# Optimization experiments

Measured on AMD Instinct MI355X. Metric: run time of the kernel, lower is better.

Reference implementation:

```python
import jax, jax.numpy as jnp
import numpy as np

HIDDEN = 1024
NUM_HEADS = 16
B, S = 2, 2048


def _mha(x, w_in, b_in, w_out, b_out, num_heads):
    # x: [..., L, E]; standard nn.MultiheadAttention math (eval mode, no dropout)
    lead = x.shape[:-2]
    L, E = x.shape[-2], x.shape[-1]
    dh = E // num_heads
    qkv = x @ w_in.T + b_in                      # [..., L, 3E]
    q, k, v = jnp.split(qkv, 3, axis=-1)
    q = q.reshape(lead + (L, num_heads, dh)) * (dh ** -0.5)
    k = k.reshape(lead + (L, num_heads, dh))
    v = v.reshape(lead + (L, num_heads, dh))
    scores = jnp.einsum('...qhd,...khd->...hqk', q, k)
    probs = jax.nn.softmax(scores, axis=-1)
    out = jnp.einsum('...hqk,...khd->...qhd', probs, v).reshape(lead + (L, E))
    return out @ w_out.T + b_out


def setup_inputs() -> dict:
    key = jax.random.key(0)
    ks = jax.random.split(key, 12)
    E = HIDDEN
    s_in = 1.0 / np.sqrt(E)
    inp = {
        'x': jax.random.normal(ks[0], (B, S, E), dtype=jnp.float32),
        'w_in_g': jax.random.normal(ks[1], (3 * E, E), dtype=jnp.float32) * s_in,
        'b_in_g': jnp.zeros((3 * E,), dtype=jnp.float32),
        'w_out_g': jax.random.normal(ks[2], (E, E), dtype=jnp.float32) * s_in,
        'b_out_g': jnp.zeros((E,), dtype=jnp.float32),
        'w_in_l': jax.random.normal(ks[3], (3 * E, E), dtype=jnp.float32) * s_in,
        'b_in_l': jnp.zeros((3 * E,), dtype=jnp.float32),
        'w_out_l': jax.random.normal(ks[4], (E, E), dtype=jnp.float32) * s_in,
        'b_out_l': jnp.zeros((E,), dtype=jnp.float32),
        'w_f': jax.random.normal(ks[5], (E, 2 * E), dtype=jnp.float32) * (1.0 / np.sqrt(2 * E)),
        'b_f': jnp.zeros((E,), dtype=jnp.float32),
    }
    return inp


def reference(x, w_in_g, b_in_g, w_out_g, b_out_g,
              w_in_l, b_in_l, w_out_l, b_out_l, w_f, b_f):
    Bn, Sn, E = x.shape
    # global full attention over the whole sequence
    g = _mha(x, w_in_g, b_in_g, w_out_g, b_out_g, NUM_HEADS)   # [B,S,E]
    # block-local attention: blocks of length num_heads along the sequence
    sub_len = NUM_HEADS
    sub_num = Sn // sub_len
    xb = x.reshape(Bn, sub_num, sub_len, E)
    l = _mha(xb, w_in_l, b_in_l, w_out_l, b_out_l, NUM_HEADS).reshape(Bn, Sn, E)
    fused = jnp.concatenate([g, l], axis=-1)                   # [B,S,2E]
    return fused @ w_f.T + b_f
```

## Files before the change

kernel.cpp:

```cpp
#include <hip/hip_runtime.h>
#include <hip/hip_bf16.h>
#include <math.h>
#include <stdint.h>

constexpr int Bz = 2;
constexpr int S  = 2048;
constexpr int E  = 1024;
constexpr int NH = 16;
constexpr int DH = 64;
constexpr int QS = 6144;
constexpr int NSPLIT = 2;
constexpr int KT_SPLIT = (S / 64) / NSPLIT;

typedef __attribute__((ext_vector_type(8))) short short8;
typedef __attribute__((ext_vector_type(4))) float f32x4;
typedef __attribute__((ext_vector_type(8))) unsigned short bf16x8;
typedef __attribute__((ext_vector_type(4))) unsigned short bf16x4;

__device__ __forceinline__ float bf2f(unsigned short u) {
    union { unsigned int i; float f; } c; c.i = ((unsigned int)u) << 16; return c.f;
}
__device__ __forceinline__ unsigned short f2bf(float f) {
    union { float f; unsigned int i; } c; c.f = f;
    unsigned int r = c.i + 0x7fffu + ((c.i >> 16) & 1u);
    return (unsigned short)(r >> 16);
}

__device__ __forceinline__ void pack4_store(unsigned short* dst,
                                            float a, float b, float c, float d) {
#if __has_builtin(__builtin_amdgcn_cvt_pk_bf16_f32)
    auto p0 = __builtin_amdgcn_cvt_pk_bf16_f32(a, b);
    auto p1 = __builtin_amdgcn_cvt_pk_bf16_f32(c, d);
    union { decltype(p0) v; unsigned int u; } c0, c1;
    c0.v = p0; c1.v = p1;
    uint2 w; w.x = c0.u; w.y = c1.u;
    *(uint2*)dst = w;
#else
    bf16x4 o = { f2bf(a), f2bf(b), f2bf(c), f2bf(d) };
    *(bf16x4*)dst = o;
#endif
}

#define GLD_LDS(g, l) __builtin_amdgcn_global_load_lds( \
    (const __attribute__((address_space(1))) void*)(g), \
    (__attribute__((address_space(3))) void*)(l), 16, 0, 0)

struct PrepArgs {
    const float* csrc[4]; unsigned short* cdst[4]; int cn[4];
    const float* wog; const float* wol;
    unsigned short* wogT; unsigned short* wolT;
    const float* wf; const float* bf; const float* bog; const float* bol;
    float* cb;
};

__global__ __launch_bounds__(256)
void prep_all(PrepArgs a)
{
    __shared__ unsigned short T[64][72];
    const int bid = blockIdx.x, t = threadIdx.x;

    if (bid < 12288) {
        int i = (bid * 256 + t) * 4;
        #pragma unroll
        for (int r = 0; r < 4; ++r) {
            if (i < a.cn[r]) {
                float4 v = *(const float4*)(a.csrc[r] + i);
                bf16x4 o = { f2bf(v.x), f2bf(v.y), f2bf(v.z), f2bf(v.w) };
                *(bf16x4*)(a.cdst[r] + i) = o;
                return;
            }
            i -= a.cn[r];
        }
        return;
    }
    if (bid < 12800) {
        const int id = bid - 12288;
        const int tj = id & 15, ti = (id >> 4) & 15, mat = id >> 8;
        const float* src = mat ? a.wol : a.wog;
        unsigned short* dst = mat ? a.wolT : a.wogT;
        #pragma unroll
        for (int r = 0; r < 4; ++r) {
            const int c = r * 256 + t;
            const int row = c >> 4, col4 = (c & 15) * 4;
            float4 v = *(const float4*)(src + (size_t)(ti * 64 + row) * 1024 + tj * 64 + col4);
            T[col4 + 0][row] = f2bf(v.x);
            T[col4 + 1][row] = f2bf(v.y);
            T[col4 + 2][row] = f2bf(v.z);
            T[col4 + 3][row] = f2bf(v.w);
        }
        __syncthreads();
        #pragma unroll
        for (int r = 0; r < 2; ++r) {
            const int c = r * 256 + t;
            const int jrow = c >> 3, ig = (c & 7) * 8;
            bf16x8 o;
            #pragma unroll
            for (int k = 0; k < 8; ++k) o[k] = T[jrow][ig + k];
            *(bf16x8*)(dst + (size_t)(tj * 64 + jrow) * 1024 + ti * 64 + ig) = o;
        }
        return;
    }
    {
        const int lane = t & 63;
        const int n = (bid - 12800) * 4 + (t >> 6);
        const float* row = a.wf + (size_t)n * 2048;
        float s = 0.f;
        #pragma unroll
        for (int i = 0; i < 16; ++i) s = fmaf(row[i * 64 + lane], a.bog[i * 64 + lane], s);
        #pragma unroll
        for (int i = 16; i < 32; ++i) s = fmaf(row[i * 64 + lane], a.bol[i * 64 + lane - 1024], s);
        #pragma unroll
        for (int off = 32; off > 0; off >>= 1) s += __shfl_xor(s, off, 64);
        if (lane == 0) a.cb[n] = a.bf[n] + s;
    }
}

__global__ __launch_bounds__(256, 2)
void gemm_bk64(const unsigned short* __restrict__ A, const unsigned short* __restrict__ W,
               const float* __restrict__ bias0, const float* __restrict__ bias1,
               unsigned short* __restrict__ C, unsigned short* __restrict__ vtout,
               unsigned short* __restrict__ vtlout,
               int M, int N, int K, int lda, int ldw, int ldc, int nsplit)
{
    __shared__ __align__(16) short As[128 * 64];
    __shared__ __align__(16) short Bs[128 * 64];
    const int t = threadIdx.x;
    const int lane = t & 63, wave = t >> 6;
    const int wm = wave & 1, wn = wave >> 1;
    const int m0 = blockIdx.y * 128, n0 = blockIdx.x * 128;
    const int lm = lane & 15, lk = lane >> 4;

    f32x4 acc[4][4] = {};

    const int row0 = t >> 3, kg0 = (t & 7) * 8;
    const unsigned short* a0 = A + (size_t)(m0 + row0) * lda + kg0;
    const unsigned short* w0 = W + (size_t)(n0 + row0) * ldw + kg0;

    for (int k0 = 0; k0 < K; k0 += 64) {
        __syncthreads();
        #pragma unroll
        for (int r = 0; r < 4; ++r)
            GLD_LDS(a0 + (size_t)(r * 32) * lda + k0, As + ((size_t)(r * 256 + wave * 64)) * 8);
        #pragma unroll
        for (int r = 0; r < 4; ++r)
            GLD_LDS(w0 + (size_t)(r * 32) * ldw + k0, Bs + ((size_t)(r * 256 + wave * 64)) * 8);
        __syncthreads();

        #pragma unroll
        for (int ks = 0; ks < 2; ++ks) {
            short8 af[4], bfr[4];
            #pragma unroll
            for (int i = 0; i < 4; ++i)
                af[i] = *(const short8*)&As[(wm * 64 + i * 16 + lm) * 64 + ks * 32 + lk * 8];
            #pragma unroll
            for (int j = 0; j < 4; ++j)
                bfr[j] = *(const short8*)&Bs[(wn * 64 + j * 16 + lm) * 64 + ks * 32 + lk * 8];
            #pragma unroll
            for (int i = 0; i < 4; ++i)
                #pragma unroll
                for (int j = 0; j < 4; ++j)
                    acc[i][j] = __builtin_amdgcn_mfma_f32_16x16x32_bf16(af[i], bfr[j], acc[i][j], 0, 0, 0);
        }
    }

    #pragma unroll
    for (int i = 0; i < 4; ++i) {
        #pragma unroll
        for (int j = 0; j < 4; ++j) {
            const int nn = n0 + wn * 64 + j * 16 + lm;
            const float bv = (nn < nsplit) ? (bias0 ? bias0[nn] : 0.f)
                                           : (bias1 ? bias1[nn - nsplit] : 0.f);
            const int mm0 = m0 + wm * 64 + i * 16 + lk * 4;
            float vv[4];
            #pragma unroll
            for (int r = 0; r < 4; ++r) {
                vv[r] = acc[i][j][r] + bv;
                C[(size_t)(mm0 + r) * ldc + nn] = f2bf(vv[r]);
            }
            if (vtout) {
                const int nl = nn - 2048;
                if (nl >= 0 && nl < 1024) {
                    const int hh = nl >> 6, dd = nl & 63;
                    const int bb = mm0 >> 11, ss = mm0 & 2047;
                    pack4_store(vtout + ((size_t)(bb * NH + hh) * 64 + dd) * S + ss,
                                vv[0], vv[1], vv[2], vv[3]);
                }
                const int nl2 = nn - 5120;
                if (nl2 >= 0) {
                    const int hh = nl2 >> 6, dd = nl2 & 63;
                    const int bb = mm0 >> 11, ss = mm0 & 2047;
                    pack4_store(vtlout + ((size_t)(bb * NH + hh) * 64 + dd) * S + ss,
                                vv[0], vv[1], vv[2], vv[3]);
                }
            }
        }
    }
}

template<typename OutT>
__global__ __launch_bounds__(256, 2)
void gemm_m64(const unsigned short* __restrict__ A, const unsigned short* __restrict__ W,
              const float* __restrict__ bias, OutT* __restrict__ C,
              int M, int N, int K, int lda, int ldw, int ldc,
              size_t sAz, size_t sWz, size_t sCz)
{
    __shared__ __align__(16) short As[64 * 32];
    __shared__ __align__(16) short Bs[128 * 32];
    const int z = blockIdx.z;
    A += z * sAz;  W += z * sWz;  C += z * sCz;

    const int t = threadIdx.x;
    const int lane = t & 63, wave = t >> 6;
    const int wm = wave & 1, wn = wave >> 1;
    const int m0 = blockIdx.y * 64, n0 = blockIdx.x * 128;
    const int lm = lane & 15, lk = lane >> 4;

    f32x4 acc[2][4] = {};

    const int rowA = t >> 2, kgA = (t & 3) * 8;
    const unsigned short* aptr = A + (size_t)(m0 + rowA) * lda + kgA;
    const unsigned short* wptr = W + (size_t)(n0 + rowA) * ldw + kgA;

    for (int k0 = 0; k0 < K; k0 += 32) {
        __syncthreads();
        GLD_LDS(aptr + k0, As + ((size_t)(wave * 64)) * 8);
        #pragma unroll
        for (int r = 0; r < 2; ++r)
            GLD_LDS(wptr + (size_t)(r * 64) * ldw + k0, Bs + ((size_t)(r * 256 + wave * 64)) * 8);
        __syncthreads();

        short8 af[2], bfr[4];
        #pragma unroll
        for (int i = 0; i < 2; ++i)
            af[i] = *(const short8*)&As[(wm * 32 + i * 16 + lm) * 32 + lk * 8];
        #pragma unroll
        for (int j = 0; j < 4; ++j)
            bfr[j] = *(const short8*)&Bs[(wn * 64 + j * 16 + lm) * 32 + lk * 8];
        #pragma unroll
        for (int i = 0; i < 2; ++i)
            #pragma unroll
            for (int j = 0; j < 4; ++j)
                acc[i][j] = __builtin_amdgcn_mfma_f32_16x16x32_bf16(af[i], bfr[j], acc[i][j], 0, 0, 0);
    }

    #pragma unroll
    for (int i = 0; i < 2; ++i) {
        #pragma unroll
        for (int j = 0; j < 4; ++j) {
            const int nn = n0 + wn * 64 + j * 16 + lm;
            const float bv = bias ? bias[nn] : 0.f;
            #pragma unroll
            for (int r = 0; r < 4; ++r) {
                const int mm = m0 + wm * 32 + i * 16 + lk * 4 + r;
                const float v = acc[i][j][r] + bv;
                const size_t idx = (size_t)mm * ldc + nn;
                if constexpr (sizeof(OutT) == 2) ((unsigned short*)C)[idx] = f2bf(v);
                else                             C[idx] = v;
            }
        }
    }
}

__global__ __launch_bounds__(256, 2)
void attn_flash(const unsigned short* __restrict__ qkv,
                const unsigned short* __restrict__ vt,
                unsigned short* __restrict__ opart, float* __restrict__ lbuf)
{
    __shared__ __align__(16) unsigned short Ks[2][64][32];
    __shared__ __align__(16) unsigned short Vs[2][64][32];
    __shared__ __align__(16) unsigned short Pt[4][2][16][64];

    const int t = threadIdx.x, lane = t & 63, wq = t >> 6;
    const int lm = lane & 15, lk = lane >> 4;
    const int bid = blockIdx.x;
    const int split = bid & 1;
    const int qb = (bid >> 1) & 15;
    const int h  = (bid >> 5) & 15;
    const int b  = bid >> 9;
    const int q0 = qb * 128 + wq * 32;

    constexpr float QSCALE = 0.125f * 1.44269504088896340736f;
    short8 qf[2][2];
    #pragma unroll
    for (int qg = 0; qg < 2; ++qg) {
        const unsigned short* qrow = qkv + ((size_t)(b * S) + q0 + qg * 16 + lm) * QS + h * DH;
        #pragma unroll
        for (int kk = 0; kk < 2; ++kk) {
            bf16x8 v = *(const bf16x8*)(qrow + kk * 32 + lk * 8);
            #pragma unroll
            for (int j = 0; j < 8; ++j)
                ((unsigned short*)&qf[qg][kk])[j] = f2bf(bf2f(v[j]) * QSCALE);
        }
    }

    short8 ones;
    #pragma unroll
    for (int j = 0; j < 8; ++j) ((unsigned short*)&ones)[j] = 0x3F80;

    const int row0 = t >> 2;
    const int sw0 = (row0 ^ (row0 >> 2)) & 3;
    const int g0 = ((t & 3) ^ sw0) * 8;
    const unsigned short* kg[2];
    const unsigned short* vg[2];
    #pragma unroll
    for (int r = 0; r < 2; ++r) {
        kg[r] = qkv + ((size_t)(b * S) + row0) * QS + E + h * 64 + r * 32 + g0;
        vg[r] = vt + ((size_t)(b * NH + h) * 64 + row0) * S + r * 32 + g0;
    }
    unsigned short* kl[2] = { &Ks[0][0][0] + (wq * 64) * 8, &Ks[0][0][0] + (256 + wq * 64) * 8 };
    unsigned short* vl[2] = { &Vs[0][0][0] + (wq * 64) * 8, &Vs[0][0][0] + (256 + wq * 64) * 8 };

    f32x4 O[2][4] = {};
    f32x4 lacc[2] = {};
    const int sw = lm & 7;
    const int fr = (lm ^ (lm >> 2)) & 3;

    for (int kt = split * KT_SPLIT; kt < (split + 1) * KT_SPLIT; ++kt) {
        __syncthreads();
        GLD_LDS(kg[0] + (size_t)kt * 64 * QS, kl[0]);
        GLD_LDS(kg[1] + (size_t)kt * 64 * QS, kl[1]);
        GLD_LDS(vg[0] + kt * 64, vl[0]);
        GLD_LDS(vg[1] + kt * 64, vl[1]);
        __syncthreads();

        f32x4 st[2][4];
        #pragma unroll
        for (int qg = 0; qg < 2; ++qg)
            #pragma unroll
            for (int jn = 0; jn < 4; ++jn)
                st[qg][jn] = (f32x4){ -16.f, -16.f, -16.f, -16.f };
        #pragma unroll
        for (int jn = 0; jn < 4; ++jn) {
            #pragma unroll
            for (int kk = 0; kk < 2; ++kk) {
                short8 kf = *(const short8*)&Ks[kk][jn * 16 + lm][(lk ^ fr) * 8];
                #pragma unroll
                for (int qg = 0; qg < 2; ++qg)
                    st[qg][jn] = __builtin_amdgcn_mfma_f32_16x16x32_bf16(kf, qf[qg][kk], st[qg][jn], 0, 0, 0);
            }
        }

        #pragma unroll
        for (int qg = 0; qg < 2; ++qg)
            #pragma unroll
            for (int jn = 0; jn < 4; ++jn) {
                const int cc = ((jn * 2 + (lk >> 1)) ^ sw) * 8 + (lk & 1) * 4;
                pack4_store(&Pt[wq][qg][lm][cc],
                            exp2f(st[qg][jn][0]), exp2f(st[qg][jn][1]),
                            exp2f(st[qg][jn][2]), exp2f(st[qg][jn][3]));
            }

        short8 pf[2][2];
        #pragma unroll
        for (int qg = 0; qg < 2; ++qg) {
            pf[qg][0] = *(const short8*)&Pt[wq][qg][lm][((lk + 0) ^ sw) * 8];
            pf[qg][1] = *(const short8*)&Pt[wq][qg][lm][((lk + 4) ^ sw) * 8];
        }

        #pragma unroll
        for (int qg = 0; qg < 2; ++qg)
            #pragma unroll
            for (int kk = 0; kk < 2; ++kk)
                lacc[qg] = __builtin_amdgcn_mfma_f32_16x16x32_bf16(ones, pf[qg][kk], lacc[qg], 0, 0, 0);

        #pragma unroll
        for (int jd = 0; jd < 4; ++jd) {
            #pragma unroll
            for (int kk = 0; kk < 2; ++kk) {
                short8 vf = *(const short8*)&Vs[kk][jd * 16 + lm][(lk ^ fr) * 8];
                #pragma unroll
                for (int qg = 0; qg < 2; ++qg)
                    O[qg][jd] = __builtin_amdgcn_mfma_f32_16x16x32_bf16(vf, pf[qg][kk], O[qg][jd], 0, 0, 0);
            }
        }
    }

    #pragma unroll
    for (int qg = 0; qg < 2; ++qg) {
        const int q = q0 + qg * 16 + lm;
        unsigned short* orow = opart + ((((size_t)split * Bz + b) * NH + h) * S + q) * 64;
        #pragma unroll
        for (int jd = 0; jd < 4; ++jd)
            pack4_store(orow + jd * 16 + lk * 4,
                        O[qg][jd][0], O[qg][jd][1], O[qg][jd][2], O[qg][jd][3]);
        if (lk == 0)
            lbuf[(((size_t)split * Bz + b) * NH + h) * S + q] = lacc[qg][0];
    }
}

__global__ __launch_bounds__(256)
void attn_merge(const unsigned short* __restrict__ opart, const float* __restrict__ lbuf,
                unsigned short* __restrict__ attn)
{
    const int id = blockIdx.x * 256 + threadIdx.x;
    const int d8 = id & 7;
    const int q  = (id >> 3) & (S - 1);
    const int h  = (id >> 14) & 15;
    const int b  = id >> 18;

    const size_t base0 = (((size_t)0 * Bz + b) * NH + h) * S + q;
    const size_t base1 = (((size_t)1 * Bz + b) * NH + h) * S + q;
    const float inv = 1.0f / (lbuf[base0] + lbuf[base1]);

    bf16x8 o0 = *(const bf16x8*)(opart + base0 * 64 + d8 * 8);
    bf16x8 o1 = *(const bf16x8*)(opart + base1 * 64 + d8 * 8);
    unsigned short* dst = attn + ((size_t)(b * S) + q) * 2048 + h * 64 + d8 * 8;
    #pragma unroll
    for (int j = 0; j < 8; j += 4)
        pack4_store(dst + j,
                    (bf2f(o0[j+0]) + bf2f(o1[j+0])) * inv,
                    (bf2f(o0[j+1]) + bf2f(o1[j+1])) * inv,
                    (bf2f(o0[j+2]) + bf2f(o1[j+2])) * inv,
                    (bf2f(o0[j+3]) + bf2f(o1[j+3])) * inv);
}

__global__ __launch_bounds__(256)
void attn_local_mfma(const unsigned short* __restrict__ qkvl,
                     const unsigned short* __restrict__ vtl,
                     unsigned short* __restrict__ outp)
{
    __shared__ __align__(16) unsigned short Pt[4][16][32];
    const int t = threadIdx.x, lane = t & 63, wq = t >> 6;
    const int lm = lane & 15, lk = lane >> 4;
    const int gid = blockIdx.x * 4 + wq;
    const int h   = gid & 15;
    const int sub = (gid >> 4) & 127;
    const int b   = gid >> 11;
    const int s0  = sub * 16;

    const unsigned short* base = qkvl + ((size_t)(b * S) + s0 + lm) * QS;
    f32x4 st = {};
    #pragma unroll
    for (int kk = 0; kk < 2; ++kk) {
        short8 kf = *(const short8*)(base + E + h * 64 + kk * 32 + lk * 8);
        short8 qf = *(const short8*)(base +     h * 64 + kk * 32 + lk * 8);
        st = __builtin_amdgcn_mfma_f32_16x16x32_bf16(kf, qf, st, 0, 0, 0);
    }

    constexpr float SC = 0.125f * 1.44269504088896340736f;
    float tt[4];
    #pragma unroll
    for (int r = 0; r < 4; ++r) tt[r] = st[r] * SC;
    float mx = fmaxf(fmaxf(tt[0], tt[1]), fmaxf(tt[2], tt[3]));
    mx = fmaxf(mx, __shfl_xor(mx, 16, 64));
    mx = fmaxf(mx, __shfl_xor(mx, 32, 64));
    float p[4], l = 0.f;
    #pragma unroll
    for (int r = 0; r < 4; ++r) { p[r] = exp2f(tt[r] - mx); l += p[r]; }
    l += __shfl_xor(l, 16, 64);
    l += __shfl_xor(l, 32, 64);
    const float inv = 1.0f / l;

    pack4_store(&Pt[wq][lm][lk * 4], p[0], p[1], p[2], p[3]);
    pack4_store(&Pt[wq][lm][16 + lk * 4], 0.f, 0.f, 0.f, 0.f);
    short8 pf = *(const short8*)&Pt[wq][lm][lk * 8];

    const unsigned short* vrow =
        vtl + (((size_t)(b * NH + h) * 64) + lm) * S + s0 + (lk & 1) * 8;
    f32x4 zero = {};
    unsigned short* dst = outp + ((size_t)(b * S) + s0 + lm) * 2048 + 1024 + h * 64 + lk * 4;
    #pragma unroll
    for (int jd = 0; jd < 4; ++jd) {
        short8 vf = *(const short8*)(vrow + (size_t)jd * 16 * S);
        f32x4 O = __builtin_amdgcn_mfma_f32_16x16x32_bf16(vf, pf, zero, 0, 0, 0);
        pack4_store(dst + jd * 16, O[0] * inv, O[1] * inv, O[2] * inv, O[3] * inv);
    }
}

extern "C" void kernel_launch(void* const* d_in, const int* in_sizes, int n_in,
                              void* d_out, int out_size, void* d_ws, size_t ws_size,
                              hipStream_t stream)
{
    const float* x       = (const float*)d_in[0];
    const float* w_in_g  = (const float*)d_in[1];
    const float* b_in_g  = (const float*)d_in[2];
    const float* w_out_g = (const float*)d_in[3];
    const float* b_out_g = (const float*)d_in[4];
    const float* w_in_l  = (const float*)d_in[5];
    const float* b_in_l  = (const float*)d_in[6];
    const float* w_out_l = (const float*)d_in[7];
    const float* b_out_l = (const float*)d_in[8];
    const float* w_f     = (const float*)d_in[9];
    const float* b_f     = (const float*)d_in[10];
    float* out = (float*)d_out;

    const int M = Bz * S;
    char* p = (char*)d_ws;
    unsigned short* xb       = (unsigned short*)p; p += (size_t)M * 1024 * 2;
    unsigned short* qkv_all  = (unsigned short*)p; p += (size_t)M * QS * 2;
    unsigned short* attn_cat = (unsigned short*)p; p += (size_t)M * 2048 * 2;
    unsigned short* win_all  = (unsigned short*)p; p += (size_t)6144 * 1024 * 2;
    unsigned short* wf_b     = (unsigned short*)p; p += (size_t)1024 * 2048 * 2;
    unsigned short* woutT    = (unsigned short*)p; p += (size_t)2 * 1024 * 1024 * 2;
    unsigned short* wcomb    = (unsigned short*)p; p += (size_t)1024 * 2048 * 2;
    unsigned short* vtbuf    = (unsigned short*)p; p += (size_t)Bz * NH * 64 * S * 2;
    unsigned short* opart    = (unsigned short*)p; p += (size_t)NSPLIT * Bz * NH * S * 64 * 2;
    float*          lbuf     = (float*)p;          p += (size_t)NSPLIT * Bz * NH * S * 4;
    float*          cb       = (float*)p;          p += 1024 * 4;

    unsigned short* vtlbuf = opart;

    dim3 blk(256);

    PrepArgs pa;
    pa.csrc[0] = x;      pa.cdst[0] = xb;                    pa.cn[0] = M * 1024;
    pa.csrc[1] = w_in_g; pa.cdst[1] = win_all;               pa.cn[1] = 3072 * 1024;
    pa.csrc[2] = w_in_l; pa.cdst[2] = win_all + 3072 * 1024; pa.cn[2] = 3072 * 1024;
    pa.csrc[3] = w_f;    pa.cdst[3] = wf_b;                  pa.cn[3] = 1024 * 2048;
    pa.wog = w_out_g; pa.wol = w_out_l;
    pa.wogT = woutT;  pa.wolT = woutT + 1024 * 1024;
    pa.wf = w_f; pa.bf = b_f; pa.bog = b_out_g; pa.bol = b_out_l; pa.cb = cb;
    prep_all<<<dim3(13056), blk, 0, stream>>>(pa);

    gemm_m64<unsigned short><<<dim3(8, 16, 2), blk, 0, stream>>>(
        wf_b, woutT, nullptr, wcomb,
        1024, 1024, 1024, 2048, 1024, 2048,
        1024, (size_t)1024 * 1024, 1024);

    gemm_bk64<<<dim3(6144 / 128, M / 128), blk, 0, stream>>>(
        xb, win_all, b_in_g, b_in_l, qkv_all, vtbuf, vtlbuf,
        M, 6144, 1024, 1024, 1024, QS, 3072);

    attn_local_mfma<<<dim3(Bz * NH * (S / 16) / 4), blk, 0, stream>>>(
        qkv_all + 3072, vtlbuf, attn_cat);

    attn_flash<<<dim3(Bz * NH * (S / 128) * NSPLIT), blk, 0, stream>>>(
        qkv_all, vtbuf, opart, lbuf);
    attn_merge<<<dim3(Bz * NH * S * 8 / 256), blk, 0, stream>>>(opart, lbuf, attn_cat);

    gemm_m64<float><<<dim3(1024 / 128, M / 64, 1), blk, 0, stream>>>(
        attn_cat, wcomb, cb, out,
        M, 1024, 2048, 2048, 2048, 1024,
        0, 0, 0);
}
```

Baseline: 312.3 us.

## Merge GEMM launches and fuse local/global attention, drop split-K merge

```diff
diff --git a/kernel.cpp b/kernel.cpp
--- a/kernel.cpp
+++ b/kernel.cpp
@@ -9,8 +9,6 @@
 constexpr int NH = 16;
 constexpr int DH = 64;
 constexpr int QS = 6144;
-constexpr int NSPLIT = 2;
-constexpr int KT_SPLIT = (S / 64) / NSPLIT;
 
 typedef __attribute__((ext_vector_type(8))) short short8;
 typedef __attribute__((ext_vector_type(4))) float f32x4;
@@ -115,19 +113,45 @@
     }
 }
 
+struct GemmFusedArgs {
+    const unsigned short* xb;    const unsigned short* win;
+    const unsigned short* wfb;   const unsigned short* woutT;
+    const float* bg;             const float* bl;
+    unsigned short* qkv;  unsigned short* vt;  unsigned short* vtl;
+    unsigned short* wcomb;
+};
+
 __global__ __launch_bounds__(256, 2)
-void gemm_bk64(const unsigned short* __restrict__ A, const unsigned short* __restrict__ W,
-               const float* __restrict__ bias0, const float* __restrict__ bias1,
-               unsigned short* __restrict__ C, unsigned short* __restrict__ vtout,
-               unsigned short* __restrict__ vtlout,
-               int M, int N, int K, int lda, int ldw, int ldc, int nsplit)
+void gemm_fused(GemmFusedArgs g)
 {
     __shared__ __align__(16) short As[128 * 64];
     __shared__ __align__(16) short Bs[128 * 64];
+
+    const int bid = blockIdx.x;
+    const unsigned short *A, *W;
+    unsigned short *C, *vt, *vtl;
+    const float *bias0, *bias1;
+    int m0, n0, lda, ldw, ldc, nsplit;
+
+    if (bid < 1536) {
+        m0 = (bid / 48) * 128;  n0 = (bid % 48) * 128;
+        A = g.xb;  W = g.win;  C = g.qkv;  vt = g.vt;  vtl = g.vtl;
+        bias0 = g.bg;  bias1 = g.bl;
+        lda = 1024;  ldw = 1024;  ldc = QS;  nsplit = 3072;
+    } else {
+        const int id = bid - 1536;
+        const int z = id >> 6;
+        m0 = ((id >> 3) & 7) * 128;  n0 = (id & 7) * 128;
+        A = g.wfb + z * 1024;
+        W = g.woutT + (size_t)z * 1024 * 1024;
+        C = g.wcomb + z * 1024;
+        vt = nullptr;  vtl = nullptr;  bias0 = nullptr;  bias1 = nullptr;
+        lda = 2048;  ldw = 1024;  ldc = 2048;  nsplit = 0;
+    }
+
     const int t = threadIdx.x;
     const int lane = t & 63, wave = t >> 6;
     const int wm = wave & 1, wn = wave >> 1;
-    const int m0 = blockIdx.y * 128, n0 = blockIdx.x * 128;
     const int lm = lane & 15, lk = lane >> 4;
 
     f32x4 acc[4][4] = {};
@@ -136,7 +160,7 @@
     const unsigned short* a0 = A + (size_t)(m0 + row0) * lda + kg0;
     const unsigned short* w0 = W + (size_t)(n0 + row0) * ldw + kg0;
 
-    for (int k0 = 0; k0 < K; k0 += 64) {
+    for (int k0 = 0; k0 < 1024; k0 += 64) {
         __syncthreads();
         #pragma unroll
         for (int r = 0; r < 4; ++r)
@@ -177,19 +201,19 @@
                 vv[r] = acc[i][j][r] + bv;
                 C[(size_t)(mm0 + r) * ldc + nn] = f2bf(vv[r]);
             }
-            if (vtout) {
+            if (vt) {
                 const int nl = nn - 2048;
                 if (nl >= 0 && nl < 1024) {
                     const int hh = nl >> 6, dd = nl & 63;
                     const int bb = mm0 >> 11, ss = mm0 & 2047;
-                    pack4_store(vtout + ((size_t)(bb * NH + hh) * 64 + dd) * S + ss,
+                    pack4_store(vt + ((size_t)(bb * NH + hh) * 64 + dd) * S + ss,
                                 vv[0], vv[1], vv[2], vv[3]);
                 }
                 const int nl2 = nn - 5120;
                 if (nl2 >= 0) {
                     const int hh = nl2 >> 6, dd = nl2 & 63;
                     const int bb = mm0 >> 11, ss = mm0 & 2047;
-                    pack4_store(vtlout + ((size_t)(bb * NH + hh) * 64 + dd) * S + ss,
+                    pack4_store(vtl + ((size_t)(bb * NH + hh) * 64 + dd) * S + ss,
                                 vv[0], vv[1], vv[2], vv[3]);
                 }
             }
@@ -262,9 +286,10 @@
 }
 
 __global__ __launch_bounds__(256, 2)
-void attn_flash(const unsigned short* __restrict__ qkv,
+void attn_fused(const unsigned short* __restrict__ qkv,
                 const unsigned short* __restrict__ vt,
-                unsigned short* __restrict__ opart, float* __restrict__ lbuf)
+                const unsigned short* __restrict__ vtl,
+                unsigned short* __restrict__ attn)
 {
     __shared__ __align__(16) unsigned short Ks[2][64][32];
     __shared__ __align__(16) unsigned short Vs[2][64][32];
@@ -272,157 +297,127 @@
 
     const int t = threadIdx.x, lane = t & 63, wq = t >> 6;
     const int lm = lane & 15, lk = lane >> 4;
-    const int bid = blockIdx.x;
-    const int split = bid & 1;
-    const int qb = (bid >> 1) & 15;
-    const int h  = (bid >> 5) & 15;
-    const int b  = bid >> 9;
-    const int q0 = qb * 128 + wq * 32;
-
-    constexpr float QSCALE = 0.125f * 1.44269504088896340736f;
-    short8 qf[2][2];
-    #pragma unroll
-    for (int qg = 0; qg < 2; ++qg) {
-        const unsigned short* qrow = qkv + ((size_t)(b * S) + q0 + qg * 16 + lm) * QS + h * DH;
-        #pragma unroll
-        for (int kk = 0; kk < 2; ++kk) {
-            bf16x8 v = *(const bf16x8*)(qrow + kk * 32 + lk * 8);
-            #pragma unroll
-            for (int j = 0; j < 8; ++j)
-                ((unsigned short*)&qf[qg][kk])[j] = f2bf(bf2f(v[j]) * QSCALE);
-        }
-    }
-
-    short8 ones;
-    #pragma unroll
-    for (int j = 0; j < 8; ++j) ((unsigned short*)&ones)[j] = 0x3F80;
-
-    const int row0 = t >> 2;
-    const int sw0 = (row0 ^ (row0 >> 2)) & 3;
-    const int g0 = ((t & 3) ^ sw0) * 8;
-    const unsigned short* kg[2];
-    const unsigned short* vg[2];
-    #pragma unroll
-    for (int r = 0; r < 2; ++r) {
-        kg[r] = qkv + ((size_t)(b * S) + row0) * QS + E + h * 64 + r * 32 + g0;
-        vg[r] = vt + ((size_t)(b * NH + h) * 64 + row0) * S + r * 32 + g0;
-    }
-    unsigned short* kl[2] = { &Ks[0][0][0] + (wq * 64) * 8, &Ks[0][0][0] + (256 + wq * 64) * 8 };
-    unsigned short* vl[2] = { &Vs[0][0][0] + (wq * 64) * 8, &Vs[0][0][0] + (256 + wq * 64) * 8 };
-
-    f32x4 O[2][4] = {};
-    f32x4 lacc[2] = {};
-    const int sw = lm & 7;
-    const int fr = (lm ^ (lm >> 2)) & 3;
-
-    for (int kt = split * KT_SPLIT; kt < (split + 1) * KT_SPLIT; ++kt) {
-        __syncthreads();
-        GLD_LDS(kg[0] + (size_t)kt * 64 * QS, kl[0]);
-        GLD_LDS(kg[1] + (size_t)kt * 64 * QS, kl[1]);
-        GLD_LDS(vg[0] + kt * 64, vl[0]);
-        GLD_LDS(vg[1] + kt * 64, vl[1]);
-        __syncthreads();
-
-        f32x4 st[2][4];
-        #pragma unroll
-        for (int qg = 0; qg < 2; ++qg)
-            #pragma unroll
-            for (int jn = 0; jn < 4; ++jn)
-                st[qg][jn] = (f32x4){ -16.f, -16.f, -16.f, -16.f };
-        #pragma unroll
-        for (int jn = 0; jn < 4; ++jn) {
+
+    if (blockIdx.x < 512) {
+        const int bid = blockIdx.x;
+        const int qb = bid & 15;
+        const int h  = (bid >> 4) & 15;
+        const int b  = bid >> 8;
+        const int q0 = qb * 128 + wq * 32;
+
+        constexpr float QSCALE = 0.125f * 1.44269504088896340736f;
+        short8 qf[2][2];
+        #pragma unroll
+        for (int qg = 0; qg < 2; ++qg) {
+            const unsigned short* qrow = qkv + ((size_t)(b * S) + q0 + qg * 16 + lm) * QS + h * DH;
             #pragma unroll
             for (int kk = 0; kk < 2; ++kk) {
-                short8 kf = *(const short8*)&Ks[kk][jn * 16 + lm][(lk ^ fr) * 8];
-                #pragma unroll
-                for (int qg = 0; qg < 2; ++qg)
-                    st[qg][jn] = __builtin_amdgcn_mfma_f32_16x16x32_bf16(kf, qf[qg][kk], st[qg][jn], 0, 0, 0);
-            }
-        }
-
-        #pragma unroll
-        for (int qg = 0; qg < 2; ++qg)
+                bf16x8 v = *(const bf16x8*)(qrow + kk * 32 + lk * 8);
+                #pragma unroll
+                for (int j = 0; j < 8; ++j)
+                    ((unsigned short*)&qf[qg][kk])[j] = f2bf(bf2f(v[j]) * QSCALE);
+            }
+        }
+
+        short8 ones;
+        #pragma unroll
+        for (int j = 0; j < 8; ++j) ((unsigned short*)&ones)[j] = 0x3F80;
+
+        const int row0 = t >> 2;
+        const int sw0 = (row0 ^ (row0 >> 2)) & 3;
+        const int g0 = ((t & 3) ^ sw0) * 8;
+        const unsigned short* kg[2];
+        const unsigned short* vg[2];
+        #pragma unroll
+        for (int r = 0; r < 2; ++r) {
+            kg[r] = qkv + ((size_t)(b * S) + row0) * QS + E + h * 64 + r * 32 + g0;
+            vg[r] = vt + ((size_t)(b * NH + h) * 64 + row0) * S + r * 32 + g0;
+        }
+        unsigned short* kl[2] = { &Ks[0][0][0] + (wq * 64) * 8, &Ks[0][0][0] + (256 + wq * 64) * 8 };
+        unsigned short* vl[2] = { &Vs[0][0][0] + (wq * 64) * 8, &Vs[0][0][0] + (256 + wq * 64) * 8 };
+
+        f32x4 O[2][4] = {};
+        f32x4 lacc[2] = {};
+        const int sw = lm & 7;
+        const int fr = (lm ^ (lm >> 2)) & 3;
+
+        for (int kt = 0; kt < 32; ++kt) {
+            __syncthreads();
+            GLD_LDS(kg[0] + (size_t)kt * 64 * QS, kl[0]);
+            GLD_LDS(kg[1] + (size_t)kt * 64 * QS, kl[1]);
+            GLD_LDS(vg[0] + kt * 64, vl[0]);
+            GLD_LDS(vg[1] + kt * 64, vl[1]);
+            __syncthreads();
+
+            f32x4 st[2][4];
+            #pragma unroll
+            for (int qg = 0; qg < 2; ++qg)
+                #pragma unroll
+                for (int jn = 0; jn < 4; ++jn)
+                    st[qg][jn] = (f32x4){ -16.f, -16.f, -16.f, -16.f };
             #pragma unroll
             for (int jn = 0; jn < 4; ++jn) {
-                const int cc = ((jn * 2 + (lk >> 1)) ^ sw) * 8 + (lk & 1) * 4;
-                pack4_store(&Pt[wq][qg][lm][cc],
-                            exp2f(st[qg][jn][0]), exp2f(st[qg][jn][1]),
-                            exp2f(st[qg][jn][2]), exp2f(st[qg][jn][3]));
-            }
-
-        short8 pf[2][2];
+                #pragma unroll
+                for (int kk = 0; kk < 2; ++kk) {
+                    short8 kf = *(const short8*)&Ks[kk][jn * 16 + lm][(lk ^ fr) * 8];
+                    #pragma unroll
+                    for (int qg = 0; qg < 2; ++qg)
+                        st[qg][jn] = __builtin_amdgcn_mfma_f32_16x16x32_bf16(kf, qf[qg][kk], st[qg][jn], 0, 0, 0);
+                }
+            }
+
+            #pragma unroll
+            for (int qg = 0; qg < 2; ++qg)
+                #pragma unroll
+                for (int jn = 0; jn < 4; ++jn) {
+                    const int cc = ((jn * 2 + (lk >> 1)) ^ sw) * 8 + (lk & 1) * 4;
+                    pack4_store(&Pt[wq][qg][lm][cc],
+                                exp2f(st[qg][jn][0]), exp2f(st[qg][jn][1]),
+                                exp2f(st[qg][jn][2]), exp2f(st[qg][jn][3]));
+                }
+
+            short8 pf[2][2];
+            #pragma unroll
+            for (int qg = 0; qg < 2; ++qg) {
+                pf[qg][0] = *(const short8*)&Pt[wq][qg][lm][((lk + 0) ^ sw) * 8];
+                pf[qg][1] = *(const short8*)&Pt[wq][qg][lm][((lk + 4) ^ sw) * 8];
+            }
+
+            #pragma unroll
+            for (int qg = 0; qg < 2; ++qg)
+                #pragma unroll
+                for (int kk = 0; kk < 2; ++kk)
+                    lacc[qg] = __builtin_amdgcn_mfma_f32_16x16x32_bf16(ones, pf[qg][kk], lacc[qg], 0, 0, 0);
+
+            #pragma unroll
+            for (int jd = 0; jd < 4; ++jd) {
+                #pragma unroll
+                for (int kk = 0; kk < 2; ++kk) {
+                    short8 vf = *(const short8*)&Vs[kk][jd * 16 + lm][(lk ^ fr) * 8];
+                    #pragma unroll
+                    for (int qg = 0; qg < 2; ++qg)
+                        O[qg][jd] = __builtin_amdgcn_mfma_f32_16x16x32_bf16(vf, pf[qg][kk], O[qg][jd], 0, 0, 0);
+                }
+            }
+        }
+
         #pragma unroll
         for (int qg = 0; qg < 2; ++qg) {
-            pf[qg][0] = *(const short8*)&Pt[wq][qg][lm][((lk + 0) ^ sw) * 8];
-            pf[qg][1] = *(const short8*)&Pt[wq][qg][lm][((lk + 4) ^ sw) * 8];
-        }
-
-        #pragma unroll
-        for (int qg = 0; qg < 2; ++qg)
-            #pragma unroll
-            for (int kk = 0; kk < 2; ++kk)
-                lacc[qg] = __builtin_amdgcn_mfma_f32_16x16x32_bf16(ones, pf[qg][kk], lacc[qg], 0, 0, 0);
-
-        #pragma unroll
-        for (int jd = 0; jd < 4; ++jd) {
-            #pragma unroll
-            for (int kk = 0; kk < 2; ++kk) {
-                short8 vf = *(const short8*)&Vs[kk][jd * 16 + lm][(lk ^ fr) * 8];
-                #pragma unroll
-                for (int qg = 0; qg < 2; ++qg)
-                    O[qg][jd] = __builtin_amdgcn_mfma_f32_16x16x32_bf16(vf, pf[qg][kk], O[qg][jd], 0, 0, 0);
-            }
-        }
-    }
-
-    #pragma unroll
-    for (int qg = 0; qg < 2; ++qg) {
-        const int q = q0 + qg * 16 + lm;
-        unsigned short* orow = opart + ((((size_t)split * Bz + b) * NH + h) * S + q) * 64;
-        #pragma unroll
-        for (int jd = 0; jd < 4; ++jd)
-            pack4_store(orow + jd * 16 + lk * 4,
-                        O[qg][jd][0], O[qg][jd][1], O[qg][jd][2], O[qg][jd][3]);
-        if (lk == 0)
-            lbuf[(((size_t)split * Bz + b) * NH + h) * S + q] = lacc[qg][0];
-    }
-}
-
-__global__ __launch_bounds__(256)
-void attn_merge(const unsigned short* __restrict__ opart, const float* __restrict__ lbuf,
-                unsigned short* __restrict__ attn)
-{
-    const int id = blockIdx.x * 256 + threadIdx.x;
-    const int d8 = id & 7;
-    const int q  = (id >> 3) & (S - 1);
-    const int h  = (id >> 14) & 15;
-    const int b  = id >> 18;
-
-    const size_t base0 = (((size_t)0 * Bz + b) * NH + h) * S + q;
-    const size_t base1 = (((size_t)1 * Bz + b) * NH + h) * S + q;
-    const float inv = 1.0f / (lbuf[base0] + lbuf[base1]);
-
-    bf16x8 o0 = *(const bf16x8*)(opart + base0 * 64 + d8 * 8);
-    bf16x8 o1 = *(const bf16x8*)(opart + base1 * 64 + d8 * 8);
-    unsigned short* dst = attn + ((size_t)(b * S) + q) * 2048 + h * 64 + d8 * 8;
-    #pragma unroll
-    for (int j = 0; j < 8; j += 4)
-        pack4_store(dst + j,
-                    (bf2f(o0[j+0]) + bf2f(o1[j+0])) * inv,
-                    (bf2f(o0[j+1]) + bf2f(o1[j+1])) * inv,
-                    (bf2f(o0[j+2]) + bf2f(o1[j+2])) * inv,
-                    (bf2f(o0[j+3]) + bf2f(o1[j+3])) * inv);
-}
-
-__global__ __launch_bounds__(256)
-void attn_local_mfma(const unsigned short* __restrict__ qkvl,
-                     const unsigned short* __restrict__ vtl,
-                     unsigned short* __restrict__ outp)
-{
-    __shared__ __align__(16) unsigned short Pt[4][16][32];
-    const int t = threadIdx.x, lane = t & 63, wq = t >> 6;
-    const int lm = lane & 15, lk = lane >> 4;
-    const int gid = blockIdx.x * 4 + wq;
+            const int q = q0 + qg * 16 + lm;
+            const float inv = 1.0f / lacc[qg][0];
+            unsigned short* dst = attn + ((size_t)(b * S) + q) * 2048 + h * 64 + lk * 4;
+            #pragma unroll
+            for (int jd = 0; jd < 4; ++jd)
+                pack4_store(dst + jd * 16,
+                            O[qg][jd][0] * inv, O[qg][jd][1] * inv,
+                            O[qg][jd][2] * inv, O[qg][jd][3] * inv);
+        }
+        return;
+    }
+
+    unsigned short (*PtL)[16][32] = (unsigned short(*)[16][32])&Pt[0][0][0][0];
+    const unsigned short* qkvl = qkv + 3072;
+    const int gid = (blockIdx.x - 512) * 4 + wq;
     const int h   = gid & 15;
     const int sub = (gid >> 4) & 127;
     const int b   = gid >> 11;
@@ -451,14 +446,14 @@
     l += __shfl_xor(l, 32, 64);
     const float inv = 1.0f / l;
 
-    pack4_store(&Pt[wq][lm][lk * 4], p[0], p[1], p[2], p[3]);
-    pack4_store(&Pt[wq][lm][16 + lk * 4], 0.f, 0.f, 0.f, 0.f);
-    short8 pf = *(const short8*)&Pt[wq][lm][lk * 8];
+    pack4_store(&PtL[wq][lm][lk * 4], p[0], p[1], p[2], p[3]);
+    pack4_store(&PtL[wq][lm][16 + lk * 4], 0.f, 0.f, 0.f, 0.f);
+    short8 pf = *(const short8*)&PtL[wq][lm][lk * 8];
 
     const unsigned short* vrow =
         vtl + (((size_t)(b * NH + h) * 64) + lm) * S + s0 + (lk & 1) * 8;
     f32x4 zero = {};
-    unsigned short* dst = outp + ((size_t)(b * S) + s0 + lm) * 2048 + 1024 + h * 64 + lk * 4;
+    unsigned short* dst = attn + ((size_t)(b * S) + s0 + lm) * 2048 + 1024 + h * 64 + lk * 4;
     #pragma unroll
     for (int jd = 0; jd < 4; ++jd) {
         short8 vf = *(const short8*)(vrow + (size_t)jd * 16 * S);
@@ -494,11 +489,8 @@
     unsigned short* woutT    = (unsigned short*)p; p += (size_t)2 * 1024 * 1024 * 2;
     unsigned short* wcomb    = (unsigned short*)p; p += (size_t)1024 * 2048 * 2;
     unsigned short* vtbuf    = (unsigned short*)p; p += (size_t)Bz * NH * 64 * S * 2;
-    unsigned short* opart    = (unsigned short*)p; p += (size_t)NSPLIT * Bz * NH * S * 64 * 2;
-    float*          lbuf     = (float*)p;          p += (size_t)NSPLIT * Bz * NH * S * 4;
+    unsigned short* vtlbuf   = (unsigned short*)p; p += (size_t)Bz * NH * 64 * S * 2;
     float*          cb       = (float*)p;          p += 1024 * 4;
-
-    unsigned short* vtlbuf = opart;
 
     dim3 blk(256);
 
@@ -512,21 +504,13 @@
     pa.wf = w_f; pa.bf = b_f; pa.bog = b_out_g; pa.bol = b_out_l; pa.cb = cb;
     prep_all<<<dim3(13056), blk, 0, stream>>>(pa);
 
-    gemm_m64<unsigned short><<<dim3(8, 16, 2), blk, 0, stream>>>(
-        wf_b, woutT, nullptr, wcomb,
-        1024, 1024, 1024, 2048, 1024, 2048,
-        1024, (size_t)1024 * 1024, 1024);
-
-    gemm_bk64<<<dim3(6144 / 128, M / 128), blk, 0, stream>>>(
-        xb, win_all, b_in_g, b_in_l, qkv_all, vtbuf, vtlbuf,
-        M, 6144, 1024, 1024, 1024, QS, 3072);
-
-    attn_local_mfma<<<dim3(Bz * NH * (S / 16) / 4), blk, 0, stream>>>(
-        qkv_all + 3072, vtlbuf, attn_cat);
-
-    attn_flash<<<dim3(Bz * NH * (S / 128) * NSPLIT), blk, 0, stream>>>(
-        qkv_all, vtbuf, opart, lbuf);
-    attn_merge<<<dim3(Bz * NH * S * 8 / 256), blk, 0, stream>>>(opart, lbuf, attn_cat);
+    GemmFusedArgs ga;
+    ga.xb = xb;  ga.win = win_all;  ga.wfb = wf_b;  ga.woutT = woutT;
+    ga.bg = b_in_g;  ga.bl = b_in_l;
+    ga.qkv = qkv_all;  ga.vt = vtbuf;  ga.vtl = vtlbuf;  ga.wcomb = wcomb;
+    gemm_fused<<<dim3(1664), blk, 0, stream>>>(ga);
+
+    attn_fused<<<dim3(1536), blk, 0, stream>>>(qkv_all, vtbuf, vtlbuf, attn_cat);
 
     gemm_m64<float><<<dim3(1024 / 128, M / 64, 1), blk, 0, stream>>>(
         attn_cat, wcomb, cb, out,
```

Result: faster. 291.7 us (-6.6%).
